# Kernel tuning notes

Measured on AMD Instinct MI355X. Metric: run time of the kernel, lower is better.

Reference implementation:

```python
import jax, jax.numpy as jnp
import numpy as np

# ---- problem sizes ----
CNO = 10000        # constant_no
PAD = 10001        # padding_idx (also used as the 'variable' marker in queries)
KS = max(CNO, PAD) + 2   # key_scale / pack_base = 10003
N_PRED = 128
F = 2_000_000
B = 200_000


def _build_segment_index(keys: np.ndarray, max_key: int):
    """numpy replica of torch _build_segment_index: (order, starts, lens)."""
    order = np.argsort(keys, kind='stable')
    uniq, counts = np.unique(keys, return_counts=True)  # unique keys, sorted
    starts = np.zeros(max_key, dtype=np.int64)
    lens = np.zeros(max_key, dtype=np.int64)
    cum = np.cumsum(counts)
    starts[uniq] = cum - counts
    lens[uniq] = counts
    return order, starts, lens


def setup_inputs() -> dict:
    rng = np.random.default_rng(0)
    # facts: [F,3] (pred, arg0, arg1), constants in [1, CNO]
    fp = rng.integers(0, N_PRED, F)
    fa0 = rng.integers(1, CNO + 1, F)
    fa1 = rng.integers(1, CNO + 1, F)
    # FactIndex.__init__ sorts facts by packed hash before building indices
    hashes = (fp.astype(np.int64) * KS + fa0) * KS + fa1
    h_order = np.argsort(hashes, kind='stable')
    fp, fa0, fa1 = fp[h_order], fa0[h_order], fa1[h_order]
    # three segment indexes: (pred,arg0), (pred,arg1), pred-only
    k0 = fp.astype(np.int64) * KS + fa0
    k1 = fp.astype(np.int64) * KS + fa1
    o0, s0, l0 = _build_segment_index(k0, int(k0.max()) + 1)
    o1, s1, l1 = _build_segment_index(k1, int(k1.max()) + 1)
    op, sp, lp = _build_segment_index(fp.astype(np.int64), int(fp.max()) + 1)
    # queries: 1/3 (pred,const,var), 1/3 (pred,var,const), 1/3 (pred,var,var)
    qp = rng.integers(0, N_PRED, B)
    pattern = rng.integers(0, 3, B)
    c0 = rng.integers(1, CNO + 1, B)
    c1 = rng.integers(1, CNO + 1, B)
    qa0 = np.where(pattern == 0, c0, PAD)
    qa1 = np.where(pattern == 1, c1, PAD)
    query_atoms = np.stack([qp, qa0, qa1], axis=1)
    ja = lambda a: jnp.asarray(a, dtype=jnp.int32)
    return {
        'query_atoms': ja(query_atoms),
        'a0_order': ja(o0), 'a0_starts': ja(s0), 'a0_lens': ja(l0),
        'a1_order': ja(o1), 'a1_starts': ja(s1), 'a1_lens': ja(l1),
        'p_order': ja(op), 'p_starts': ja(sp), 'p_lens': ja(lp),
        'max_results': 64,
    }


def reference(query_atoms, a0_order, a0_starts, a0_lens,
              a1_order, a1_starts, a1_lens,
              p_order, p_starts, p_lens, max_results):
    B = query_atoms.shape[0]
    F = a0_order.shape[0]
    clamp_max = max(F - 1, 0)
    preds = query_atoms[:, 0]
    a0 = query_atoms[:, 1]
    a1 = query_atoms[:, 2]
    is_c0 = (a0 <= CNO) & (a0 != PAD)
    is_c1 = (a1 <= CNO) & (a1 != PAD)
    offsets = jnp.arange(max_results, dtype=jnp.int32)[None, :]  # [1,K]

    def _lookup(order, starts, lens, keys, is_const):
        safe = jnp.clip(keys, 0, starts.shape[0] - 1)
        left = starts[safe]                                  # [B]
        cnt = jnp.minimum(lens[safe], max_results)           # [B]
        idx = jnp.clip(left[:, None] + offsets, 0, clamp_max)  # [B,K]
        v = (offsets < cnt[:, None]) & is_const[:, None]
        return order[idx], v

    fi0, v0 = _lookup(a0_order, a0_starts, a0_lens, preds * KS + a0, is_c0)
    fi1, v1 = _lookup(a1_order, a1_starts, a1_lens, preds * KS + a1, is_c1)
    use0 = is_c0[:, None]
    fact_idx = jnp.where(use0, fi0, fi1)
    valid = jnp.where(use0, v0, v1)
    # pred-only fallback when both args are variables
    both_var = (~is_c0) & (~is_c1) & (preds != PAD)
    fip, vp = _lookup(p_order, p_starts, p_lens, preds, both_var)
    bv = both_var[:, None]
    fact_idx = jnp.where(bv, fip, fact_idx)
    valid = jnp.where(bv, vp, valid)
    return fact_idx, valid
```

## Files before the change

kernel.cpp:

```cpp
#include <hip/hip_runtime.h>

#define CNO_C 10000
#define PAD_C 10001
#define KS_C  10003

typedef int iv4 __attribute__((ext_vector_type(4)));

__global__ __launch_bounds__(256) void akfi_vec8(
    const int* __restrict__ qa,
    const int* __restrict__ o0, const int* __restrict__ s0, const int* __restrict__ l0,
    const int* __restrict__ o1, const int* __restrict__ s1, const int* __restrict__ l1,
    const int* __restrict__ op, const int* __restrict__ sp, const int* __restrict__ lp,
    int n0, int n1, int npred,
    int F, int B,
    int* __restrict__ out_idx,
    int* __restrict__ out_valid)
{
    long long t = (long long)blockIdx.x * blockDim.x + threadIdx.x;
    long long total = (long long)B * 8;
    if (t >= total) return;

    int q  = (int)(t >> 3);
    int j8 = (int)(t & 7) << 3;

    int p  = qa[q * 3 + 0];
    int a0 = qa[q * 3 + 1];
    int a1 = qa[q * 3 + 2];

    bool is_c0 = (a0 <= CNO_C) && (a0 != PAD_C);
    bool is_c1 = (a1 <= CNO_C) && (a1 != PAD_C);
    bool both  = (!is_c0) && (!is_c1) && (p != PAD_C);

    const int* order; const int* starts; const int* lens;
    int key, nsz; bool isc;
    if (is_c0)      { order = o0; starts = s0; lens = l0; key = p * KS_C + a0; nsz = n0;    isc = true;  }
    else if (both)  { order = op; starts = sp; lens = lp; key = p;             nsz = npred; isc = true;  }
    else            { order = o1; starts = s1; lens = l1; key = p * KS_C + a1; nsz = n1;    isc = is_c1; }

    int safe = min(max(key, 0), nsz - 1);
    int left = starts[safe];
    int cnt  = min(lens[safe], 64);
    if (!isc) cnt = 0;
    const int Fm1 = F - 1;

    int idx0 = left + j8;
    int f[8];
    if (idx0 >= 0 && idx0 + 7 <= Fm1) {
#pragma unroll
        for (int e = 0; e < 8; ++e) f[e] = order[idx0 + e];
    } else {
#pragma unroll
        for (int e = 0; e < 8; ++e) f[e] = order[min(max(idx0 + e, 0), Fm1)];
    }

    iv4 fv0 = (iv4){f[0], f[1], f[2], f[3]};
    iv4 fv1 = (iv4){f[4], f[5], f[6], f[7]};
    iv4 vv0 = (iv4){j8     < cnt ? 1 : 0, j8 + 1 < cnt ? 1 : 0,
                    j8 + 2 < cnt ? 1 : 0, j8 + 3 < cnt ? 1 : 0};
    iv4 vv1 = (iv4){j8 + 4 < cnt ? 1 : 0, j8 + 5 < cnt ? 1 : 0,
                    j8 + 6 < cnt ? 1 : 0, j8 + 7 < cnt ? 1 : 0};

    long long ob = ((long long)q << 6) + j8;
    *reinterpret_cast<iv4*>(out_idx + ob)       = fv0;
    *reinterpret_cast<iv4*>(out_idx + ob + 4)   = fv1;
    *reinterpret_cast<iv4*>(out_valid + ob)     = vv0;
    *reinterpret_cast<iv4*>(out_valid + ob + 4) = vv1;
}

__global__ __launch_bounds__(256) void akfi_vec4(
    const int* __restrict__ qa,
    const int* __restrict__ o0, const int* __restrict__ s0, const int* __restrict__ l0,
    const int* __restrict__ o1, const int* __restrict__ s1, const int* __restrict__ l1,
    const int* __restrict__ op, const int* __restrict__ sp, const int* __restrict__ lp,
    int n0, int n1, int npred,
    int F, int B, int mr,
    int* __restrict__ out_idx,
    int* __restrict__ out_valid)
{
    long long t = (long long)blockIdx.x * blockDim.x + threadIdx.x;
    int per_q = mr >> 2;
    long long total = (long long)B * per_q;
    if (t >= total) return;

    int q = (int)(t / per_q), j4 = (int)(t % per_q) << 2;

    int p  = qa[q * 3 + 0];
    int a0 = qa[q * 3 + 1];
    int a1 = qa[q * 3 + 2];
    bool is_c0 = (a0 <= CNO_C) && (a0 != PAD_C);
    bool is_c1 = (a1 <= CNO_C) && (a1 != PAD_C);
    bool both  = (!is_c0) && (!is_c1) && (p != PAD_C);

    const int* order; const int* starts; const int* lens;
    int key, nsz; bool isc;
    if (is_c0)      { order = o0; starts = s0; lens = l0; key = p * KS_C + a0; nsz = n0;    isc = true;  }
    else if (both)  { order = op; starts = sp; lens = lp; key = p;             nsz = npred; isc = true;  }
    else            { order = o1; starts = s1; lens = l1; key = p * KS_C + a1; nsz = n1;    isc = is_c1; }

    int safe = min(max(key, 0), nsz - 1);
    int left = starts[safe];
    int cnt  = min(lens[safe], mr);
    if (!isc) cnt = 0;
    int Fm1 = F - 1;

    int idx0 = left + j4;
    int f0, f1, f2, f3;
    if (idx0 >= 0 && idx0 + 3 <= Fm1) {
        f0 = order[idx0]; f1 = order[idx0 + 1]; f2 = order[idx0 + 2]; f3 = order[idx0 + 3];
    } else {
        f0 = order[min(max(idx0,     0), Fm1)];
        f1 = order[min(max(idx0 + 1, 0), Fm1)];
        f2 = order[min(max(idx0 + 2, 0), Fm1)];
        f3 = order[min(max(idx0 + 3, 0), Fm1)];
    }

    iv4 fv = (iv4){f0, f1, f2, f3};
    iv4 vv = (iv4){j4 < cnt ? 1 : 0, j4 + 1 < cnt ? 1 : 0,
                   j4 + 2 < cnt ? 1 : 0, j4 + 3 < cnt ? 1 : 0};
    long long ob = (long long)q * mr + j4;
    *reinterpret_cast<iv4*>(out_idx + ob)   = fv;
    *reinterpret_cast<iv4*>(out_valid + ob) = vv;
}

__global__ __launch_bounds__(256) void akfi_scalar(
    const int* __restrict__ qa,
    const int* __restrict__ o0, const int* __restrict__ s0, const int* __restrict__ l0,
    const int* __restrict__ o1, const int* __restrict__ s1, const int* __restrict__ l1,
    const int* __restrict__ op, const int* __restrict__ sp, const int* __restrict__ lp,
    int n0, int n1, int npred,
    int F, int B, int mr,
    int* __restrict__ out_idx,
    int* __restrict__ out_valid)
{
    long long t = (long long)blockIdx.x * blockDim.x + threadIdx.x;
    long long total = (long long)B * (long long)mr;
    if (t >= total) return;
    int q = (int)(t / mr), j = (int)(t % mr);

    int p  = qa[q * 3 + 0];
    int a0 = qa[q * 3 + 1];
    int a1 = qa[q * 3 + 2];
    bool is_c0 = (a0 <= CNO_C) && (a0 != PAD_C);
    bool is_c1 = (a1 <= CNO_C) && (a1 != PAD_C);
    bool both  = (!is_c0) && (!is_c1) && (p != PAD_C);

    const int* order; const int* starts; const int* lens;
    int key, nsz; bool isc;
    if (is_c0)      { order = o0; starts = s0; lens = l0; key = p * KS_C + a0; nsz = n0;    isc = true;  }
    else if (both)  { order = op; starts = sp; lens = lp; key = p;             nsz = npred; isc = true;  }
    else            { order = o1; starts = s1; lens = l1; key = p * KS_C + a1; nsz = n1;    isc = is_c1; }

    int safe = min(max(key, 0), nsz - 1);
    int left = starts[safe];
    int cnt  = min(lens[safe], mr);
    int idx  = min(max(left + j, 0), F - 1);

    long long ob = (long long)q * mr + j;
    out_idx[ob]   = order[idx];
    out_valid[ob] = (isc && j < cnt) ? 1 : 0;
}

extern "C" void kernel_launch(void* const* d_in, const int* in_sizes, int n_in,
                              void* d_out, int out_size, void* d_ws, size_t ws_size,
                              hipStream_t stream) {
    const int* qa = (const int*)d_in[0];
    const int* o0 = (const int*)d_in[1];
    const int* s0 = (const int*)d_in[2];
    const int* l0 = (const int*)d_in[3];
    const int* o1 = (const int*)d_in[4];
    const int* s1 = (const int*)d_in[5];
    const int* l1 = (const int*)d_in[6];
    const int* op = (const int*)d_in[7];
    const int* sp = (const int*)d_in[8];
    const int* lp = (const int*)d_in[9];
    int B  = in_sizes[0] / 3;
    int F  = in_sizes[1];
    int n0 = in_sizes[2];
    int n1 = in_sizes[5];
    int npred = in_sizes[8];
    int mr = out_size / (2 * B);

    int* out_idx   = (int*)d_out;
    int* out_valid = (int*)d_out + (long long)B * mr;

    int block = 256;
    if (mr == 64) {
        long long total = (long long)B * 8;
        int blocks = (int)((total + block - 1) / block);
        akfi_vec8<<<blocks, block, 0, stream>>>(
            qa, o0, s0, l0, o1, s1, l1, op, sp, lp,
            n0, n1, npred, F, B, out_idx, out_valid);
    } else if ((mr & 3) == 0) {
        long long total = (long long)B * (mr >> 2);
        int blocks = (int)((total + block - 1) / block);
        akfi_vec4<<<blocks, block, 0, stream>>>(
            qa, o0, s0, l0, o1, s1, l1, op, sp, lp,
            n0, n1, npred, F, B, mr, out_idx, out_valid);
    } else {
        long long total = (long long)B * (long long)mr;
        int blocks = (int)((total + block - 1) / block);
        akfi_scalar<<<blocks, block, 0, stream>>>(
            qa, o0, s0, l0, o1, s1, l1, op, sp, lp,
            n0, n1, npred, F, B, mr, out_idx, out_valid);
    }
}
```

Measured before the change: 33.40 us.

## Process two queries per 16-thread group with 4-wide outputs each

Replaces the 8-elements-per-thread kernel with one where each 16-thread group handles a pair of queries, each thread writing 4 contiguous results for both queries. Each wavefront store instruction then covers contiguous 256-byte rows per query rather than strided 32-byte chunks, and two independent gather chains run per thread for more memory-level parallelism. The thread count stays the same, but each thread now does two index lookups and adds branches for the odd-B tail.

```diff
diff --git a/kernel.cpp b/kernel.cpp
--- a/kernel.cpp
+++ b/kernel.cpp
@@ -6,7 +6,7 @@
 
 typedef int iv4 __attribute__((ext_vector_type(4)));
 
-__global__ __launch_bounds__(256) void akfi_vec8(
+__global__ __launch_bounds__(256) void akfi_dual4(
     const int* __restrict__ qa,
     const int* __restrict__ o0, const int* __restrict__ s0, const int* __restrict__ l0,
     const int* __restrict__ o1, const int* __restrict__ s1, const int* __restrict__ l1,
@@ -17,54 +17,85 @@
     int* __restrict__ out_valid)
 {
     long long t = (long long)blockIdx.x * blockDim.x + threadIdx.x;
-    long long total = (long long)B * 8;
+    int npair = (B + 1) >> 1;
+    long long total = (long long)npair * 16;
     if (t >= total) return;
 
-    int q  = (int)(t >> 3);
-    int j8 = (int)(t & 7) << 3;
-
-    int p  = qa[q * 3 + 0];
-    int a0 = qa[q * 3 + 1];
-    int a1 = qa[q * 3 + 2];
-
-    bool is_c0 = (a0 <= CNO_C) && (a0 != PAD_C);
-    bool is_c1 = (a1 <= CNO_C) && (a1 != PAD_C);
-    bool both  = (!is_c0) && (!is_c1) && (p != PAD_C);
-
-    const int* order; const int* starts; const int* lens;
-    int key, nsz; bool isc;
-    if (is_c0)      { order = o0; starts = s0; lens = l0; key = p * KS_C + a0; nsz = n0;    isc = true;  }
-    else if (both)  { order = op; starts = sp; lens = lp; key = p;             nsz = npred; isc = true;  }
-    else            { order = o1; starts = s1; lens = l1; key = p * KS_C + a1; nsz = n1;    isc = is_c1; }
-
-    int safe = min(max(key, 0), nsz - 1);
-    int left = starts[safe];
-    int cnt  = min(lens[safe], 64);
-    if (!isc) cnt = 0;
+    int u  = (int)(t >> 4);
+    int j4 = (int)(t & 15) << 2;
+    int q0 = u << 1;
+    int q1 = q0 + 1;
+    bool has1 = (q1 < B);
     const int Fm1 = F - 1;
 
-    int idx0 = left + j8;
-    int f[8];
-    if (idx0 >= 0 && idx0 + 7 <= Fm1) {
-#pragma unroll
-        for (int e = 0; e < 8; ++e) f[e] = order[idx0 + e];
+    const int* qp = qa + q0 * 3;
+    int p0  = qp[0], a00 = qp[1], a01 = qp[2];
+    int p1  = has1 ? qp[3] : 0;
+    int a10 = has1 ? qp[4] : PAD_C;
+    int a11 = has1 ? qp[5] : PAD_C;
+
+    bool c0_is0 = (a00 <= CNO_C) && (a00 != PAD_C);
+    bool c0_is1 = (a01 <= CNO_C) && (a01 != PAD_C);
+    bool c0_bo  = (!c0_is0) && (!c0_is1) && (p0 != PAD_C);
+    const int *ord0, *st0, *ln0; int key0, nsz0; bool isc0;
+    if (c0_is0)     { ord0 = o0; st0 = s0; ln0 = l0; key0 = p0 * KS_C + a00; nsz0 = n0;    isc0 = true;   }
+    else if (c0_bo) { ord0 = op; st0 = sp; ln0 = lp; key0 = p0;              nsz0 = npred; isc0 = true;   }
+    else            { ord0 = o1; st0 = s1; ln0 = l1; key0 = p0 * KS_C + a01; nsz0 = n1;    isc0 = c0_is1; }
+
+    bool c1_is0 = (a10 <= CNO_C) && (a10 != PAD_C);
+    bool c1_is1 = (a11 <= CNO_C) && (a11 != PAD_C);
+    bool c1_bo  = (!c1_is0) && (!c1_is1) && (p1 != PAD_C);
+    const int *ord1, *st1, *ln1; int key1, nsz1; bool isc1;
+    if (c1_is0)     { ord1 = o0; st1 = s0; ln1 = l0; key1 = p1 * KS_C + a10; nsz1 = n0;    isc1 = true;   }
+    else if (c1_bo) { ord1 = op; st1 = sp; ln1 = lp; key1 = p1;              nsz1 = npred; isc1 = true;   }
+    else            { ord1 = o1; st1 = s1; ln1 = l1; key1 = p1 * KS_C + a11; nsz1 = n1;    isc1 = c1_is1; }
+
+    int safe0 = min(max(key0, 0), nsz0 - 1);
+    int safe1 = min(max(key1, 0), nsz1 - 1);
+    int left0 = st0[safe0];
+    int left1 = has1 ? st1[safe1] : 0;
+    int cnt0  = ln0[safe0];
+    int cnt1  = has1 ? ln1[safe1] : 0;
+    cnt0 = min(cnt0, 64); if (!isc0) cnt0 = 0;
+    cnt1 = min(cnt1, 64); if (!isc1) cnt1 = 0;
+
+    int i00 = left0 + j4;
+    int i10 = left1 + j4;
+    int g00, g01, g02, g03, g10, g11, g12, g13;
+    if (i00 >= 0 && i00 + 3 <= Fm1) {
+        g00 = ord0[i00]; g01 = ord0[i00 + 1]; g02 = ord0[i00 + 2]; g03 = ord0[i00 + 3];
     } else {
-#pragma unroll
-        for (int e = 0; e < 8; ++e) f[e] = order[min(max(idx0 + e, 0), Fm1)];
-    }
-
-    iv4 fv0 = (iv4){f[0], f[1], f[2], f[3]};
-    iv4 fv1 = (iv4){f[4], f[5], f[6], f[7]};
-    iv4 vv0 = (iv4){j8     < cnt ? 1 : 0, j8 + 1 < cnt ? 1 : 0,
-                    j8 + 2 < cnt ? 1 : 0, j8 + 3 < cnt ? 1 : 0};
-    iv4 vv1 = (iv4){j8 + 4 < cnt ? 1 : 0, j8 + 5 < cnt ? 1 : 0,
-                    j8 + 6 < cnt ? 1 : 0, j8 + 7 < cnt ? 1 : 0};
-
-    long long ob = ((long long)q << 6) + j8;
-    *reinterpret_cast<iv4*>(out_idx + ob)       = fv0;
-    *reinterpret_cast<iv4*>(out_idx + ob + 4)   = fv1;
-    *reinterpret_cast<iv4*>(out_valid + ob)     = vv0;
-    *reinterpret_cast<iv4*>(out_valid + ob + 4) = vv1;
+        g00 = ord0[min(max(i00,     0), Fm1)];
+        g01 = ord0[min(max(i00 + 1, 0), Fm1)];
+        g02 = ord0[min(max(i00 + 2, 0), Fm1)];
+        g03 = ord0[min(max(i00 + 3, 0), Fm1)];
+    }
+    if (has1) {
+        if (i10 >= 0 && i10 + 3 <= Fm1) {
+            g10 = ord1[i10]; g11 = ord1[i10 + 1]; g12 = ord1[i10 + 2]; g13 = ord1[i10 + 3];
+        } else {
+            g10 = ord1[min(max(i10,     0), Fm1)];
+            g11 = ord1[min(max(i10 + 1, 0), Fm1)];
+            g12 = ord1[min(max(i10 + 2, 0), Fm1)];
+            g13 = ord1[min(max(i10 + 3, 0), Fm1)];
+        }
+    } else { g10 = g11 = g12 = g13 = 0; }
+
+    iv4 fv0 = (iv4){g00, g01, g02, g03};
+    iv4 vv0 = (iv4){j4 < cnt0 ? 1 : 0, j4 + 1 < cnt0 ? 1 : 0,
+                    j4 + 2 < cnt0 ? 1 : 0, j4 + 3 < cnt0 ? 1 : 0};
+    long long ob0 = ((long long)q0 << 6) + j4;
+    *reinterpret_cast<iv4*>(out_idx + ob0)   = fv0;
+    *reinterpret_cast<iv4*>(out_valid + ob0) = vv0;
+
+    if (has1) {
+        iv4 fv1 = (iv4){g10, g11, g12, g13};
+        iv4 vv1 = (iv4){j4 < cnt1 ? 1 : 0, j4 + 1 < cnt1 ? 1 : 0,
+                        j4 + 2 < cnt1 ? 1 : 0, j4 + 3 < cnt1 ? 1 : 0};
+        long long ob1 = ((long long)q1 << 6) + j4;
+        *reinterpret_cast<iv4*>(out_idx + ob1)   = fv1;
+        *reinterpret_cast<iv4*>(out_valid + ob1) = vv1;
+    }
 }
 
 __global__ __launch_bounds__(256) void akfi_vec4(
@@ -185,9 +216,9 @@
 
     int block = 256;
     if (mr == 64) {
-        long long total = (long long)B * 8;
+        long long total = (long long)((B + 1) >> 1) * 16;
         int blocks = (int)((total + block - 1) / block);
-        akfi_vec8<<<blocks, block, 0, stream>>>(
+        akfi_dual4<<<blocks, block, 0, stream>>>(
             qa, o0, s0, l0, o1, s1, l1, op, sp, lp,
             n0, n1, npred, F, B, out_idx, out_valid);
     } else if ((mr & 3) == 0) {
```

New measurement: 32.00 us. -4.2%, faster.
